# Performance work log

Hardware: AMD Instinct MI355X
Metric: run time of the kernel (lower is better)

## Reference

```python
import jax, jax.numpy as jnp
import numpy as np

L, N, C = 128, 32, 128
DIM_MLP, OUT = 128, 128


def setup_inputs() -> dict:
    key = jax.random.key(0)
    ks = jax.random.split(key, 6)
    s_in2 = 1.0 / np.sqrt(2 * C)
    s_mid = 1.0 / np.sqrt(DIM_MLP)
    s_in = 1.0 / np.sqrt(C)
    return {
        "x": jax.random.normal(ks[0], (L, N, C), jnp.float32),
        "attn_w1": jax.random.normal(ks[1], (2 * C, DIM_MLP), jnp.float32) * s_in2,
        "attn_b1": jnp.zeros((DIM_MLP,), jnp.float32),
        "attn_w2": jax.random.normal(ks[2], (DIM_MLP, OUT), jnp.float32) * s_mid,
        "attn_b2": jnp.zeros((OUT,), jnp.float32),
        "value_w1": jax.random.normal(ks[3], (C, DIM_MLP), jnp.float32) * s_in,
        "value_b1": jnp.zeros((DIM_MLP,), jnp.float32),
        "value_w2": jax.random.normal(ks[4], (DIM_MLP, OUT), jnp.float32) * s_mid,
        "value_b2": jnp.zeros((OUT,), jnp.float32),
    }


def reference(x, attn_w1, attn_b1, attn_w2, attn_b2,
              value_w1, value_b1, value_w2, value_b2):
    l, n, c = x.shape
    # Outer concat: pair[i, j, b] = concat(x[i, b], x[j, b])  -> (l, l, N, 2C)
    xi = jnp.broadcast_to(x[:, None, :, :], (l, l, n, c))
    xj = jnp.broadcast_to(x[None, :, :, :], (l, l, n, c))
    pair = jnp.concatenate([xi, xj], axis=-1)
    # Pairwise attention MLP (ReLU hidden, linear output)
    h = jax.nn.relu(pair @ attn_w1 + attn_b1)          # (l, l, N, dim_mlp)
    attn = h @ attn_w2 + attn_b2                       # (l, l, N, out)
    # Value MLP
    hv = jax.nn.relu(x @ value_w1 + value_b1)          # (l, N, dim_mlp)
    value = hv @ value_w2 + value_b2                   # (l, N, out)
    # Elementwise weighted reduce over key axis j (NOT a matmul over channels)
    out = jnp.einsum('ijbc,jbc->ibc', attn, value)     # (l, N, out)
    return out
```

## Files before the change

kernel.cpp:

```cpp
#include <hip/hip_runtime.h>
#include <hip/hip_bf16.h>

#define L_DIM 128
#define N_DIM 32
#define C_DIM 128
#define K_DIM 128
#define OUT_DIM 128

typedef __attribute__((ext_vector_type(8))) short short8;
typedef __attribute__((ext_vector_type(4))) float float4v;

static __device__ __forceinline__ short bf16_bits(float f) {
    __bf16 h = (__bf16)f;
    return __builtin_bit_cast(short, h);
}

__global__ __launch_bounds__(256) void k_pre(
    const float* __restrict__ x,
    const float* __restrict__ attn_w1, const float* __restrict__ attn_b1,
    const float* __restrict__ attn_w2,
    const float* __restrict__ value_w1, const float* __restrict__ value_b1,
    const float* __restrict__ value_w2, const float* __restrict__ value_b2,
    float* __restrict__ P, float* __restrict__ Q, float* __restrict__ V,
    short* __restrict__ W2s)
{
    int bid = blockIdx.x;
    int tid = threadIdx.x;
    if (bid >= 256) {
        int e = (bid - 256) * 256 + tid;
        int idx  = e & 7;
        int colr = (e >> 3) & 15;
        int quad = (e >> 7) & 3;
        int mi   = (e >> 9) & 3;
        int ct   = e >> 11;
        int k = quad * 8 + 32 * mi + idx;
        int c = ct * 16 + colr;
        W2s[e] = bf16_bits(attn_w2[k * OUT_DIM + c]);
        return;
    }

    __shared__ float xs[16][C_DIM];
    __shared__ float W_lds[3][32][K_DIM];
    __shared__ float hvs[16][K_DIM];

    int r0 = bid * 16;

    #pragma unroll
    for (int t = 0; t < 2; ++t) {
        int e4 = t * 256 + tid;
        int row = e4 >> 5, c4 = (e4 & 31) * 4;
        *(float4v*)&xs[row][c4] = *(const float4v*)(x + (r0 + row) * C_DIM + c4);
    }

    int ks   = tid & 127;
    int half = tid >> 7;

    float pa[8] = {0,0,0,0,0,0,0,0};
    float qa[8] = {0,0,0,0,0,0,0,0};
    float ha[8] = {0,0,0,0,0,0,0,0};

    for (int ct4 = 0; ct4 < 4; ++ct4) {
        #pragma unroll
        for (int t = 0; t < 4; ++t) {
            int e4 = t * 256 + tid;
            int cc = e4 >> 5, k4 = (e4 & 31) * 4;
            *(float4v*)&W_lds[0][cc][k4] =
                *(const float4v*)(attn_w1 + (ct4 * 32 + cc) * K_DIM + k4);
            *(float4v*)&W_lds[1][cc][k4] =
                *(const float4v*)(attn_w1 + (C_DIM + ct4 * 32 + cc) * K_DIM + k4);
            *(float4v*)&W_lds[2][cc][k4] =
                *(const float4v*)(value_w1 + (ct4 * 32 + cc) * K_DIM + k4);
        }
        __syncthreads();

        for (int g = 0; g < 8; ++g) {
            float4v xr4[8];
            #pragma unroll
            for (int r = 0; r < 8; ++r)
                xr4[r] = *(const float4v*)&xs[half * 8 + r][ct4 * 32 + g * 4];
            #pragma unroll
            for (int u = 0; u < 4; ++u) {
                int cc = g * 4 + u;
                float wa = W_lds[0][cc][ks];
                float wb = W_lds[1][cc][ks];
                float wv = W_lds[2][cc][ks];
                #pragma unroll
                for (int r = 0; r < 8; ++r) {
                    float xr = xr4[r][u];
                    pa[r] = fmaf(xr, wa, pa[r]);
                    qa[r] = fmaf(xr, wb, qa[r]);
                    ha[r] = fmaf(xr, wv, ha[r]);
                }
            }
        }
        __syncthreads();
    }

    float b1 = attn_b1[ks], vb1 = value_b1[ks];
    #pragma unroll
    for (int r = 0; r < 8; ++r) {
        int rr = r0 + half * 8 + r;
        int i = rr >> 5, b = rr & 31;
        P[(b * L_DIM + i) * K_DIM + ks] = pa[r];
        Q[(b * L_DIM + i) * K_DIM + ks] = qa[r] + b1;
        hvs[half * 8 + r][ks] = fmaxf(ha[r] + vb1, 0.f);
    }

    float va[8] = {0,0,0,0,0,0,0,0};
    for (int kt = 0; kt < 4; ++kt) {
        #pragma unroll
        for (int t = 0; t < 4; ++t) {
            int e4 = t * 256 + tid;
            int cc = e4 >> 5, k4 = (e4 & 31) * 4;
            *(float4v*)&W_lds[0][cc][k4] =
                *(const float4v*)(value_w2 + (kt * 32 + cc) * OUT_DIM + k4);
        }
        __syncthreads();
        for (int g = 0; g < 8; ++g) {
            float4v hv4[8];
            #pragma unroll
            for (int r = 0; r < 8; ++r)
                hv4[r] = *(const float4v*)&hvs[half * 8 + r][kt * 32 + g * 4];
            #pragma unroll
            for (int u = 0; u < 4; ++u) {
                float w = W_lds[0][g * 4 + u][ks];
                #pragma unroll
                for (int r = 0; r < 8; ++r)
                    va[r] = fmaf(hv4[r][u], w, va[r]);
            }
        }
        __syncthreads();
    }
    float vb2 = value_b2[ks];
    #pragma unroll
    for (int r = 0; r < 8; ++r) {
        int rr = r0 + half * 8 + r;
        int i = rr >> 5, b = rr & 31;
        V[(b * L_DIM + i) * OUT_DIM + ks] = va[r] + vb2;
    }
}

#define QSTR 132

__global__ __launch_bounds__(256)
__attribute__((amdgpu_waves_per_eu(2, 2)))
void k_main(
    const float* __restrict__ P, const float* __restrict__ Q,
    const float* __restrict__ V,
    const short* __restrict__ W2s, const float* __restrict__ attn_b2,
    float* __restrict__ out)
{
    __shared__ float Qb[2][16 * QSTR];
    __shared__ float comb[4 * 8 * 64];

    int b     = blockIdx.x >> 5;
    int itile = blockIdx.x & 31;
    int tid   = threadIdx.x;
    int wave  = tid >> 6;
    int lane  = tid & 63;
    int quad  = lane >> 4;
    int col   = lane & 15;
    int ipair = wave & 1;
    int khalf = wave >> 1;
    int i0    = itile * 4 + ipair * 2;

    short8 bfrag[8][2];
    const short8* w2p = (const short8*)W2s;
    #pragma unroll
    for (int ct = 0; ct < 8; ++ct)
        #pragma unroll
        for (int mi = 0; mi < 2; ++mi)
            bfrag[ct][mi] = w2p[((ct * 4 + (khalf * 2 + mi)) * 4 + quad) * 16 + col];

    float4v p[2][2][2];
    #pragma unroll
    for (int il = 0; il < 2; ++il) {
        const float* Pr = P + (b * L_DIM + i0 + il) * K_DIM;
        #pragma unroll
        for (int mi = 0; mi < 2; ++mi) {
            int k0 = quad * 8 + (khalf * 2 + mi) * 32;
            p[il][mi][0] = *(const float4v*)(Pr + k0);
            p[il][mi][1] = *(const float4v*)(Pr + k0 + 4);
        }
    }

    int srow = tid >> 5;
    int sc4  = (tid & 31) * 4;
    const float* Qbase = Q + (size_t)(b * L_DIM) * K_DIM;
    const float* Vbase = V + (size_t)(b * L_DIM) * OUT_DIM;

    *(float4v*)&Qb[0][srow * QSTR + sc4] =
        *(const float4v*)(Qbase + srow * K_DIM + sc4);
    *(float4v*)&Qb[0][(srow + 8) * QSTR + sc4] =
        *(const float4v*)(Qbase + (srow + 8) * K_DIM + sc4);
    __syncthreads();

    float acc[2][8] = {};
    float sv[8]     = {};

    #pragma unroll 1
    for (int r = 0; r < 8; ++r) {
        int cur = r & 1;

        float4v nq0, nq1;
        if (r < 7) {
            const float* qp = Qbase + (r + 1) * 16 * K_DIM;
            nq0 = *(const float4v*)(qp + srow * K_DIM + sc4);
            nq1 = *(const float4v*)(qp + (srow + 8) * K_DIM + sc4);
        }

        const float* Vr = Vbase + (r * 16 + quad * 4) * OUT_DIM + col;
        float vv[32];
        #pragma unroll
        for (int rr = 0; rr < 4; ++rr)
            #pragma unroll
            for (int ct = 0; ct < 8; ++ct)
                vv[rr * 8 + ct] = Vr[rr * OUT_DIM + ct * 16];

        short8 af[2][2];
        #pragma unroll
        for (int mi = 0; mi < 2; ++mi) {
            const float* qc = &Qb[cur][col * QSTR + quad * 8 + (khalf * 2 + mi) * 32];
            float4v q0 = *(const float4v*)qc;
            float4v q1 = *(const float4v*)(qc + 4);
            #pragma unroll
            for (int il = 0; il < 2; ++il) {
                short8 a;
                #pragma unroll
                for (int t = 0; t < 4; ++t) {
                    a[t]     = bf16_bits(fmaxf(p[il][mi][0][t] + q0[t], 0.f));
                    a[t + 4] = bf16_bits(fmaxf(p[il][mi][1][t] + q1[t], 0.f));
                }
                af[il][mi] = a;
            }
        }

        #pragma unroll
        for (int ct = 0; ct < 8; ++ct) {
            #pragma unroll
            for (int il = 0; il < 2; ++il) {
                float4v c4 = {0.f, 0.f, 0.f, 0.f};
                c4 = __builtin_amdgcn_mfma_f32_16x16x32_bf16(
                        af[il][0], bfrag[ct][0], c4, 0, 0, 0);
                c4 = __builtin_amdgcn_mfma_f32_16x16x32_bf16(
                        af[il][1], bfrag[ct][1], c4, 0, 0, 0);
                #pragma unroll
                for (int rr = 0; rr < 4; ++rr)
                    acc[il][ct] = fmaf(c4[rr], vv[rr * 8 + ct], acc[il][ct]);
            }
            if (khalf) {
                #pragma unroll
                for (int rr = 0; rr < 4; ++rr)
                    sv[ct] += vv[rr * 8 + ct];
            }
        }

        if (r < 7) {
            *(float4v*)&Qb[cur ^ 1][srow * QSTR + sc4]       = nq0;
            *(float4v*)&Qb[cur ^ 1][(srow + 8) * QSTR + sc4] = nq1;
        }
        __syncthreads();
    }

    if (khalf == 0) {
        #pragma unroll
        for (int il = 0; il < 2; ++il)
            #pragma unroll
            for (int ct = 0; ct < 8; ++ct)
                comb[((ipair * 2 + il) * 8 + ct) * 64 + lane] = acc[il][ct];
    }
    __syncthreads();
    if (khalf == 1) {
        #pragma unroll
        for (int il = 0; il < 2; ++il) {
            #pragma unroll
            for (int ct = 0; ct < 8; ++ct) {
                float tot = acc[il][ct] +
                            comb[((ipair * 2 + il) * 8 + ct) * 64 + lane];
                tot = fmaf(attn_b2[ct * 16 + col], sv[ct], tot);
                tot += __shfl_xor(tot, 16, 64);
                tot += __shfl_xor(tot, 32, 64);
                if (quad == 0)
                    out[((i0 + il) * N_DIM + b) * OUT_DIM + ct * 16 + col] = tot;
            }
        }
    }
}

extern "C" void kernel_launch(void* const* d_in, const int* in_sizes, int n_in,
                              void* d_out, int out_size, void* d_ws, size_t ws_size,
                              hipStream_t stream)
{
    const float* x        = (const float*)d_in[0];
    const float* attn_w1  = (const float*)d_in[1];
    const float* attn_b1  = (const float*)d_in[2];
    const float* attn_w2  = (const float*)d_in[3];
    const float* attn_b2  = (const float*)d_in[4];
    const float* value_w1 = (const float*)d_in[5];
    const float* value_b1 = (const float*)d_in[6];
    const float* value_w2 = (const float*)d_in[7];
    const float* value_b2 = (const float*)d_in[8];
    float* out = (float*)d_out;

    float* ws  = (float*)d_ws;
    float* P   = ws;
    float* Q   = ws + 524288;
    float* V   = ws + 1048576;
    short* W2s = (short*)(ws + 1572864);

    k_pre<<<320, 256, 0, stream>>>(x, attn_w1, attn_b1, attn_w2,
                                   value_w1, value_b1, value_w2, value_b2,
                                   P, Q, V, W2s);
    k_main<<<1024, 256, 0, stream>>>(P, Q, V, W2s, attn_b2, out);
}
```

Baseline: 130.7 us.

## Split k_main across 8 waves by column tiles, store P as bf16

```diff
diff --git a/kernel.cpp b/kernel.cpp
--- a/kernel.cpp
+++ b/kernel.cpp
@@ -13,6 +13,9 @@
 static __device__ __forceinline__ short bf16_bits(float f) {
     __bf16 h = (__bf16)f;
     return __builtin_bit_cast(short, h);
+}
+static __device__ __forceinline__ float bf16_to_f32(short s) {
+    return __builtin_bit_cast(float, ((unsigned)(unsigned short)s) << 16);
 }
 
 __global__ __launch_bounds__(256) void k_pre(
@@ -21,8 +24,8 @@
     const float* __restrict__ attn_w2,
     const float* __restrict__ value_w1, const float* __restrict__ value_b1,
     const float* __restrict__ value_w2, const float* __restrict__ value_b2,
-    float* __restrict__ P, float* __restrict__ Q, float* __restrict__ V,
-    short* __restrict__ W2s)
+    unsigned short* __restrict__ Pb, float* __restrict__ Q,
+    float* __restrict__ V, short* __restrict__ W2s)
 {
     int bid = blockIdx.x;
     int tid = threadIdx.x;
@@ -101,7 +104,7 @@
     for (int r = 0; r < 8; ++r) {
         int rr = r0 + half * 8 + r;
         int i = rr >> 5, b = rr & 31;
-        P[(b * L_DIM + i) * K_DIM + ks] = pa[r];
+        Pb[(b * L_DIM + i) * K_DIM + ks] = (unsigned short)bf16_bits(pa[r]);
         Q[(b * L_DIM + i) * K_DIM + ks] = qa[r] + b1;
         hvs[half * 8 + r][ks] = fmaxf(ha[r] + vb1, 0.f);
     }
@@ -142,149 +145,125 @@
 
 #define QSTR 132
 
-__global__ __launch_bounds__(256)
-__attribute__((amdgpu_waves_per_eu(2, 2)))
-void k_main(
-    const float* __restrict__ P, const float* __restrict__ Q,
-    const float* __restrict__ V,
-    const short* __restrict__ W2s, const float* __restrict__ attn_b2,
-    float* __restrict__ out)
+__global__ __launch_bounds__(512) void k_main(
+    const unsigned short* __restrict__ Pb, const float* __restrict__ Q,
+    const float* __restrict__ V, const short* __restrict__ W2s,
+    const float* __restrict__ attn_b2, float* __restrict__ out)
 {
     __shared__ float Qb[2][16 * QSTR];
-    __shared__ float comb[4 * 8 * 64];
-
-    int b     = blockIdx.x >> 5;
-    int itile = blockIdx.x & 31;
+
+    int blk   = blockIdx.x;
+    int b     = blk & 31;
+    int itile = blk >> 5;
     int tid   = threadIdx.x;
     int wave  = tid >> 6;
     int lane  = tid & 63;
     int quad  = lane >> 4;
     int col   = lane & 15;
     int ipair = wave & 1;
-    int khalf = wave >> 1;
+    int cquad = wave >> 1;
     int i0    = itile * 4 + ipair * 2;
-
-    short8 bfrag[8][2];
+    int ct0   = cquad * 2;
+
+    short8 bfrag[2][4];
     const short8* w2p = (const short8*)W2s;
     #pragma unroll
-    for (int ct = 0; ct < 8; ++ct)
-        #pragma unroll
-        for (int mi = 0; mi < 2; ++mi)
-            bfrag[ct][mi] = w2p[((ct * 4 + (khalf * 2 + mi)) * 4 + quad) * 16 + col];
-
-    float4v p[2][2][2];
+    for (int c2 = 0; c2 < 2; ++c2)
+        #pragma unroll
+        for (int mi = 0; mi < 4; ++mi)
+            bfrag[c2][mi] = w2p[(((ct0 + c2) * 4 + mi) * 4 + quad) * 16 + col];
+
+    short8 pb[2][4];
     #pragma unroll
     for (int il = 0; il < 2; ++il) {
-        const float* Pr = P + (b * L_DIM + i0 + il) * K_DIM;
-        #pragma unroll
-        for (int mi = 0; mi < 2; ++mi) {
-            int k0 = quad * 8 + (khalf * 2 + mi) * 32;
-            p[il][mi][0] = *(const float4v*)(Pr + k0);
-            p[il][mi][1] = *(const float4v*)(Pr + k0 + 4);
-        }
+        const unsigned short* pr = Pb + (size_t)(b * L_DIM + i0 + il) * K_DIM;
+        #pragma unroll
+        for (int mi = 0; mi < 4; ++mi)
+            pb[il][mi] = *(const short8*)(pr + quad * 8 + mi * 32);
     }
 
     int srow = tid >> 5;
     int sc4  = (tid & 31) * 4;
-    const float* Qbase = Q + (size_t)(b * L_DIM) * K_DIM;
-    const float* Vbase = V + (size_t)(b * L_DIM) * OUT_DIM;
+    const float* Qbase = Q + (size_t)b * L_DIM * K_DIM;
+    const float* Vbase = V + (size_t)b * L_DIM * OUT_DIM;
 
     *(float4v*)&Qb[0][srow * QSTR + sc4] =
         *(const float4v*)(Qbase + srow * K_DIM + sc4);
-    *(float4v*)&Qb[0][(srow + 8) * QSTR + sc4] =
-        *(const float4v*)(Qbase + (srow + 8) * K_DIM + sc4);
     __syncthreads();
 
-    float acc[2][8] = {};
-    float sv[8]     = {};
-
-    #pragma unroll 1
+    float acc[2][2] = {};
+    float sv[2]     = {};
+
     for (int r = 0; r < 8; ++r) {
         int cur = r & 1;
 
-        float4v nq0, nq1;
-        if (r < 7) {
-            const float* qp = Qbase + (r + 1) * 16 * K_DIM;
-            nq0 = *(const float4v*)(qp + srow * K_DIM + sc4);
-            nq1 = *(const float4v*)(qp + (srow + 8) * K_DIM + sc4);
-        }
-
-        const float* Vr = Vbase + (r * 16 + quad * 4) * OUT_DIM + col;
-        float vv[32];
-        #pragma unroll
-        for (int rr = 0; rr < 4; ++rr)
-            #pragma unroll
-            for (int ct = 0; ct < 8; ++ct)
-                vv[rr * 8 + ct] = Vr[rr * OUT_DIM + ct * 16];
-
-        short8 af[2][2];
-        #pragma unroll
-        for (int mi = 0; mi < 2; ++mi) {
-            const float* qc = &Qb[cur][col * QSTR + quad * 8 + (khalf * 2 + mi) * 32];
+        float4v nq;
+        if (r < 7)
+            nq = *(const float4v*)(Qbase + ((r + 1) * 16 + srow) * K_DIM + sc4);
+
+        const float* Vr = Vbase + (r * 16 + quad * 4) * OUT_DIM;
+        float vv[2][4];
+        #pragma unroll
+        for (int c2 = 0; c2 < 2; ++c2)
+            #pragma unroll
+            for (int rr = 0; rr < 4; ++rr)
+                vv[c2][rr] = Vr[rr * OUT_DIM + (ct0 + c2) * 16 + col];
+
+        float4v c4[2][2] = {};
+        #pragma unroll
+        for (int mi = 0; mi < 4; ++mi) {
+            const float* qc = &Qb[cur][col * QSTR + quad * 8 + mi * 32];
             float4v q0 = *(const float4v*)qc;
             float4v q1 = *(const float4v*)(qc + 4);
             #pragma unroll
             for (int il = 0; il < 2; ++il) {
+                float4v p0, p1;
+                #pragma unroll
+                for (int t = 0; t < 4; ++t) {
+                    p0[t] = bf16_to_f32(pb[il][mi][t]);
+                    p1[t] = bf16_to_f32(pb[il][mi][t + 4]);
+                }
+                float4v h0 = __builtin_elementwise_max(p0 + q0, (float4v)0.f);
+                float4v h1 = __builtin_elementwise_max(p1 + q1, (float4v)0.f);
                 short8 a;
                 #pragma unroll
                 for (int t = 0; t < 4; ++t) {
-                    a[t]     = bf16_bits(fmaxf(p[il][mi][0][t] + q0[t], 0.f));
-                    a[t + 4] = bf16_bits(fmaxf(p[il][mi][1][t] + q1[t], 0.f));
+                    a[t]     = bf16_bits(h0[t]);
+                    a[t + 4] = bf16_bits(h1[t]);
                 }
-                af[il][mi] = a;
-            }
-        }
-
-        #pragma unroll
-        for (int ct = 0; ct < 8; ++ct) {
-            #pragma unroll
-            for (int il = 0; il < 2; ++il) {
-                float4v c4 = {0.f, 0.f, 0.f, 0.f};
-                c4 = __builtin_amdgcn_mfma_f32_16x16x32_bf16(
-                        af[il][0], bfrag[ct][0], c4, 0, 0, 0);
-                c4 = __builtin_amdgcn_mfma_f32_16x16x32_bf16(
-                        af[il][1], bfrag[ct][1], c4, 0, 0, 0);
-                #pragma unroll
-                for (int rr = 0; rr < 4; ++rr)
-                    acc[il][ct] = fmaf(c4[rr], vv[rr * 8 + ct], acc[il][ct]);
-            }
-            if (khalf) {
-                #pragma unroll
-                for (int rr = 0; rr < 4; ++rr)
-                    sv[ct] += vv[rr * 8 + ct];
-            }
-        }
-
-        if (r < 7) {
-            *(float4v*)&Qb[cur ^ 1][srow * QSTR + sc4]       = nq0;
-            *(float4v*)&Qb[cur ^ 1][(srow + 8) * QSTR + sc4] = nq1;
-        }
-        __syncthreads();
-    }
-
-    if (khalf == 0) {
-        #pragma unroll
-        for (int il = 0; il < 2; ++il)
-            #pragma unroll
-            for (int ct = 0; ct < 8; ++ct)
-                comb[((ipair * 2 + il) * 8 + ct) * 64 + lane] = acc[il][ct];
-    }
-    __syncthreads();
-    if (khalf == 1) {
-        #pragma unroll
-        for (int il = 0; il < 2; ++il) {
-            #pragma unroll
-            for (int ct = 0; ct < 8; ++ct) {
-                float tot = acc[il][ct] +
-                            comb[((ipair * 2 + il) * 8 + ct) * 64 + lane];
-                tot = fmaf(attn_b2[ct * 16 + col], sv[ct], tot);
-                tot += __shfl_xor(tot, 16, 64);
-                tot += __shfl_xor(tot, 32, 64);
-                if (quad == 0)
-                    out[((i0 + il) * N_DIM + b) * OUT_DIM + ct * 16 + col] = tot;
-            }
-        }
-    }
+                #pragma unroll
+                for (int c2 = 0; c2 < 2; ++c2)
+                    c4[il][c2] = __builtin_amdgcn_mfma_f32_16x16x32_bf16(
+                        a, bfrag[c2][mi], c4[il][c2], 0, 0, 0);
+            }
+        }
+
+        #pragma unroll
+        for (int c2 = 0; c2 < 2; ++c2)
+            #pragma unroll
+            for (int rr = 0; rr < 4; ++rr) {
+                float v = vv[c2][rr];
+                acc[0][c2] = fmaf(c4[0][c2][rr], v, acc[0][c2]);
+                acc[1][c2] = fmaf(c4[1][c2][rr], v, acc[1][c2]);
+                sv[c2] += v;
+            }
+
+        if (r < 7)
+            *(float4v*)&Qb[cur ^ 1][srow * QSTR + sc4] = nq;
+        __syncthreads();
+    }
+
+    #pragma unroll
+    for (int il = 0; il < 2; ++il)
+        #pragma unroll
+        for (int c2 = 0; c2 < 2; ++c2) {
+            int cc = (ct0 + c2) * 16 + col;
+            float tot = fmaf(attn_b2[cc], sv[c2], acc[il][c2]);
+            tot += __shfl_xor(tot, 16, 64);
+            tot += __shfl_xor(tot, 32, 64);
+            if (quad == 0)
+                out[((i0 + il) * N_DIM + b) * OUT_DIM + cc] = tot;
+        }
 }
 
 extern "C" void kernel_launch(void* const* d_in, const int* in_sizes, int n_in,
@@ -302,14 +281,14 @@
     const float* value_b2 = (const float*)d_in[8];
     float* out = (float*)d_out;
 
-    float* ws  = (float*)d_ws;
-    float* P   = ws;
-    float* Q   = ws + 524288;
-    float* V   = ws + 1048576;
-    short* W2s = (short*)(ws + 1572864);
+    float* ws = (float*)d_ws;
+    float* Q  = ws;
+    float* V  = ws + 524288;
+    unsigned short* Pbuf = (unsigned short*)(ws + 1048576);
+    short* W2s = (short*)(ws + 1310720);
 
     k_pre<<<320, 256, 0, stream>>>(x, attn_w1, attn_b1, attn_w2,
                                    value_w1, value_b1, value_w2, value_b2,
-                                   P, Q, V, W2s);
-    k_main<<<1024, 256, 0, stream>>>(P, Q, V, W2s, attn_b2, out);
-}
+                                   Pbuf, Q, V, W2s);
+    k_main<<<1024, 512, 0, stream>>>(Pbuf, Q, V, W2s, attn_b2, out);
+}
```

Result: slower. 141.0 us (+7.9%).
